# Performance work log

Measured on AMD Instinct MI355X. Metric: run time of the kernel, lower is better.

Reference implementation:

```python
import jax, jax.numpy as jnp
from jax import lax
import numpy as np

B, T, I, H, C = 32, 256, 128, 128, 100


def setup_inputs() -> dict:
    key = jax.random.key(0)
    ks = jax.random.split(key, 9)
    s = 1.0 / np.sqrt(H)  # PyTorch LSTMCell init range
    inp = {
        "x": jax.random.normal(ks[0], (B, T, I), dtype=jnp.float32),
        "w_ih": jax.random.uniform(ks[1], (4 * H, I), jnp.float32, -s, s),
        "b_ih": jax.random.uniform(ks[2], (4 * H,), jnp.float32, -s, s),
        "w_hh": jax.random.uniform(ks[3], (4 * H, H), jnp.float32, -s, s),
        "b_hh": jax.random.uniform(ks[4], (4 * H,), jnp.float32, -s, s),
        # attention params: normal(mean=0, std=0.01) per the source
        "w1": 0.01 * jax.random.normal(ks[5], (2 * H, H), dtype=jnp.float32),
        "w2": 0.01 * jax.random.normal(ks[6], (H, 1), dtype=jnp.float32),
        "w_fc": jax.random.uniform(ks[7], (C, H), jnp.float32, -s, s),
        "b_fc": jax.random.uniform(ks[8], (C,), jnp.float32, -s, s),
    }
    return inp


def _forward(x, w_ih, b_ih, w_hh, b_hh, w1, w2, w_fc, b_fc):
    Bv, Tv, _ = x.shape
    Hv = w_hh.shape[1]
    h0 = jnp.zeros((Bv, Hv), x.dtype)
    c0 = jnp.zeros((Bv, Hv), x.dtype)
    # memory buffer: slot 0 holds the initial zero hidden state (as in the
    # torch code, h_old starts as h_t=0); slots 1..T filled as we go.
    # Unwritten (future) slots are zero, so their attn contribution
    # attn_w * h_old is exactly zero -> no mask needed, matching the
    # growing-memory semantics of the original loop.
    mem0 = jnp.zeros((Bv, Tv + 1, Hv), x.dtype)
    attn0 = jnp.zeros((Bv, Hv), x.dtype)

    def step(carry, inp):
        h, c, mem, _ = carry
        x_t, i = inp
        # PyTorch LSTMCell: gate order i, f, g, o
        gates = x_t @ w_ih.T + b_ih + h @ w_hh.T + b_hh
        ig, fg, gg, og = jnp.split(gates, 4, axis=-1)
        c = jax.nn.sigmoid(fg) * c + jax.nn.sigmoid(ig) * jnp.tanh(gg)
        h = jax.nn.sigmoid(og) * jnp.tanh(c)
        # additive attention scores over the memory (NO softmax in source)
        h_rep = jnp.broadcast_to(h[:, None, :], mem.shape)  # [B, T+1, H]
        cat = jnp.concatenate([h_rep, mem], axis=-1)        # [B, T+1, 2H]
        s = jnp.tanh(cat @ w1) @ w2                          # [B, T+1, 1]
        attn_c = jnp.sum(s * mem, axis=1)                    # [B, H]
        mem = mem.at[:, i + 1, :].set(h)  # append h_t to memory
        return (h, c, mem, attn_c), None

    xs = (jnp.transpose(x, (1, 0, 2)), jnp.arange(Tv))
    (h, c, mem, attn_c), _ = lax.scan(step, (h0, c0, mem0, attn0), xs)
    return (h + attn_c) @ w_fc.T + b_fc


def reference(x, w_ih, b_ih, w_hh, b_hh, w1, w2, w_fc, b_fc):
    return _forward(x, w_ih, b_ih, w_hh, b_hh, w1, w2, w_fc, b_fc)
```

## Files before the change

kernel.cpp:

```cpp
#include <hip/hip_runtime.h>
#include <hip/hip_bf16.h>


#define Bsz 32
#define Tsz 256
#define Isz 128
#define Hsz 128
#define Csz 100
#define G4H 512

typedef short v8s __attribute__((ext_vector_type(8)));
typedef float v4fa __attribute__((ext_vector_type(4)));

__device__ __forceinline__ float2 pk_fma(float2 a, float2 b, float2 c) {
    float2 d;
    asm("v_pk_fma_f32 %0, %1, %2, %3" : "=v"(d) : "v"(a), "v"(b), "v"(c));
    return d;
}
__device__ __forceinline__ float quad_rsum(float x) {
    int t = __builtin_amdgcn_update_dpp(0, __float_as_int(x), 0xB1, 0xF, 0xF, true);
    x += __int_as_float(t);
    t = __builtin_amdgcn_update_dpp(0, __float_as_int(x), 0x4E, 0xF, 0xF, true);
    x += __int_as_float(t);
    return x;
}
__device__ __forceinline__ float rcpf(float x) { return __builtin_amdgcn_rcpf(x); }
__device__ __forceinline__ float sigm_n(float x) { return rcpf(1.0f + __expf(-x)); }
__device__ __forceinline__ float tanh_n(float x) {
    float ax = fabsf(x);
    float e = __expf(-2.0f * ax);
    float t = (1.0f - e) * rcpf(1.0f + e);
    return copysignf(t, x);
}
__device__ __forceinline__ float tanh_s(float x) { return tanh_n(x); }
__device__ __forceinline__ short bf16_bits(float x) {
    __hip_bfloat16 h = __float2bfloat16(x);
    return *reinterpret_cast<short*>(&h);
}
__device__ __forceinline__ float bf16_val(float x) {
    return __bfloat162float(__float2bfloat16(x));
}

__global__ __launch_bounds__(256) void prep_kernel(
    const float* __restrict__ w_ih, const float* __restrict__ b_ih,
    const float* __restrict__ w_hh, const float* __restrict__ b_hh,
    const float* __restrict__ w1,
    __hip_bfloat16* __restrict__ W2ih, __hip_bfloat16* __restrict__ W2v,
    float* __restrict__ whh_pk, float* __restrict__ bias,
    float* __restrict__ attn_c) {
    int idx = blockIdx.x * blockDim.x + threadIdx.x;
    if (idx < G4H * Isz) {
        int n = idx >> 7;
        int k = idx & 127;
        float x = w_ih[idx];
        __hip_bfloat16 hi = __float2bfloat16(x);
        __hip_bfloat16 lo = __float2bfloat16(x - __bfloat162float(hi));
        W2ih[(size_t)n * 384 + k] = hi;
        W2ih[(size_t)n * 384 + 128 + k] = lo;
        W2ih[(size_t)n * 384 + 256 + k] = hi;

        int j4  = idx & 3;
        int q   = (idx >> 2) & 3;
        int d   = (idx >> 4) & 127;
        int gi  = (idx >> 11) & 3;
        int kk4 = (idx >> 13) & 7;
        whh_pk[idx] = w_hh[(size_t)((gi << 7) + d) * 128 + (q << 5) + (kk4 << 2) + j4];
    }
    if (idx < Hsz * Hsz) {
        int n = idx >> 7;
        int k = idx & 127;
        float x = w1[(size_t)(128 + k) * Hsz + n];
        __hip_bfloat16 hi = __float2bfloat16(x);
        __hip_bfloat16 lo = __float2bfloat16(x - __bfloat162float(hi));
        W2v[(size_t)n * 384 + k] = hi;
        W2v[(size_t)n * 384 + 128 + k] = lo;
        W2v[(size_t)n * 384 + 256 + k] = hi;
    }
    if (idx < G4H) bias[idx] = b_ih[idx] + b_hh[idx];
    if (idx < Bsz * Hsz) attn_c[idx] = 0.0f;
}

__global__ __launch_bounds__(256) void gemm_mfma_f32a(
    const float* __restrict__ A, const __hip_bfloat16* __restrict__ W2,
    const float* __restrict__ bias, float* __restrict__ C, int M, int N) {
    const int tid = threadIdx.x;
    const int w = tid >> 6, lane = tid & 63;
    const int m0 = blockIdx.y * 64 + (w & 1) * 32;
    const int n0 = blockIdx.x * 64 + (w >> 1) * 32;
    const int r = lane & 15, quad = lane >> 4;

    v8s Ahi[2][4], Alo[2][4];
    #pragma unroll
    for (int i = 0; i < 2; ++i)
        #pragma unroll
        for (int cb = 0; cb < 4; ++cb) {
            const float* src = A + (size_t)(m0 + 16 * i + r) * Isz + cb * 32 + quad * 8;
            float4 f0 = *(const float4*)src;
            float4 f1 = *(const float4*)(src + 4);
            float f[8] = {f0.x, f0.y, f0.z, f0.w, f1.x, f1.y, f1.z, f1.w};
            v8s hi, lo;
            #pragma unroll
            for (int e = 0; e < 8; ++e) {
                float hv = bf16_val(f[e]);
                hi[e] = bf16_bits(f[e]);
                lo[e] = bf16_bits(f[e] - hv);
            }
            Ahi[i][cb] = hi;
            Alo[i][cb] = lo;
        }

    v4fa acc[2][2] = {};
    const short* Wb = (const short*)W2;
    #pragma unroll
    for (int ks = 0; ks < 12; ++ks) {
        int cb = ks & 3;
        v8s a0 = (ks >= 8) ? Alo[0][cb] : Ahi[0][cb];
        v8s a1 = (ks >= 8) ? Alo[1][cb] : Ahi[1][cb];
        int kb = ks * 32 + quad * 8;
        v8s b0 = *(const v8s*)(Wb + (size_t)(n0 + r) * 384 + kb);
        v8s b1 = *(const v8s*)(Wb + (size_t)(n0 + 16 + r) * 384 + kb);
        acc[0][0] = __builtin_amdgcn_mfma_f32_16x16x32_bf16(a0, b0, acc[0][0], 0, 0, 0);
        acc[0][1] = __builtin_amdgcn_mfma_f32_16x16x32_bf16(a0, b1, acc[0][1], 0, 0, 0);
        acc[1][0] = __builtin_amdgcn_mfma_f32_16x16x32_bf16(a1, b0, acc[1][0], 0, 0, 0);
        acc[1][1] = __builtin_amdgcn_mfma_f32_16x16x32_bf16(a1, b1, acc[1][1], 0, 0, 0);
    }
    #pragma unroll
    for (int i = 0; i < 2; ++i)
        #pragma unroll
        for (int j = 0; j < 2; ++j) {
            int cn = n0 + 16 * j + r;
            float bb = bias ? bias[cn] : 0.0f;
            #pragma unroll
            for (int rr = 0; rr < 4; ++rr) {
                int row = m0 + 16 * i + quad * 4 + rr;
                C[(size_t)row * N + cn] = acc[i][j][rr] + bb;
            }
        }
}

#define HPAD(k) ((k) + 8 * ((k) >> 5))

__global__ __launch_bounds__(512, 2) void lstm_seq(
    const float* __restrict__ G, const float* __restrict__ whh_pk,
    float* __restrict__ H_all) {
    const int b = blockIdx.x;
    const int tid = threadIdx.x;
    const int d = tid >> 2;
    const int q = tid & 3;

    __shared__ float h_s[2][160];

    float2 w2v[4][16];
    {
        const float4* wp = (const float4*)whh_pk;
        #pragma unroll
        for (int kk4 = 0; kk4 < 8; ++kk4)
            #pragma unroll
            for (int gi = 0; gi < 4; ++gi) {
                float4 v = wp[((kk4 * 4 + gi) * 128 + d) * 4 + q];
                w2v[gi][kk4 * 2]     = make_float2(v.x, v.y);
                w2v[gi][kk4 * 2 + 1] = make_float2(v.z, v.w);
            }
    }

    if (tid < 320) ((float*)h_s)[tid] = 0.0f;
    float c = 0.0f;
    __syncthreads();

    const float* Gq = G + (size_t)b * Tsz * G4H + q * 128 + d;
    float* Hst = H_all + (size_t)b * Tsz * Hsz + d;

    float gval = Gq[0];
    int cur = 0;
    for (int t = 0; t < Tsz; ++t) {
        const int tn = (t < Tsz - 1) ? t + 1 : t;
        float ngval = Gq[(size_t)tn * G4H];

        float2 accA[4], accB[4];
        #pragma unroll
        for (int gi = 0; gi < 4; ++gi) {
            accA[gi] = make_float2(q == gi ? gval : 0.f, 0.f);
            accB[gi] = make_float2(0.f, 0.f);
        }
        const float4* hb4 = (const float4*)&h_s[cur][q * 40];
        #pragma unroll
        for (int kk4 = 0; kk4 < 8; ++kk4) {
            float4 h4 = hb4[kk4];
            float2 hA = make_float2(h4.x, h4.y);
            float2 hB = make_float2(h4.z, h4.w);
            accA[0] = pk_fma(hA, w2v[0][2 * kk4], accA[0]);
            accA[1] = pk_fma(hA, w2v[1][2 * kk4], accA[1]);
            accA[2] = pk_fma(hA, w2v[2][2 * kk4], accA[2]);
            accA[3] = pk_fma(hA, w2v[3][2 * kk4], accA[3]);
            accB[0] = pk_fma(hB, w2v[0][2 * kk4 + 1], accB[0]);
            accB[1] = pk_fma(hB, w2v[1][2 * kk4 + 1], accB[1]);
            accB[2] = pk_fma(hB, w2v[2][2 * kk4 + 1], accB[2]);
            accB[3] = pk_fma(hB, w2v[3][2 * kk4 + 1], accB[3]);
        }
        float a0 = quad_rsum(accA[0].x + accA[0].y + accB[0].x + accB[0].y);
        float a1 = quad_rsum(accA[1].x + accA[1].y + accB[1].x + accB[1].y);
        float a2 = quad_rsum(accA[2].x + accA[2].y + accB[2].x + accB[2].y);
        float a3 = quad_rsum(accA[3].x + accA[3].y + accB[3].x + accB[3].y);

        float iv = sigm_n(a0);
        float fv = sigm_n(a1);
        float gv = tanh_n(a2);
        float ov = sigm_n(a3);
        c = fv * c + iv * gv;
        float h = ov * tanh_n(c);

        if (q == 0) {
            h_s[cur ^ 1][HPAD(d)] = h;
            Hst[(size_t)t * Hsz] = h;
        }
        gval = ngval;
        __syncthreads();
        cur ^= 1;
    }
}

__global__ __launch_bounds__(256) void scores_part(
    const float* __restrict__ H_all, const float* __restrict__ KV,
    const float* __restrict__ w1, const float* __restrict__ w2,
    float* __restrict__ attn_c) {
    const int b = blockIdx.y, jt = blockIdx.x;
    const int tid = threadIdx.x;
    __shared__ float hT[Hsz];
    __shared__ float q_s[Hsz];
    __shared__ float w2s[Hsz];
    __shared__ float s_s[64];
    __shared__ float part[2][Hsz];

    const float* Hb = H_all + (size_t)b * Tsz * Hsz;
    const float* KVb = KV + (size_t)b * Tsz * Hsz;

    if (tid < Hsz) {
        hT[tid] = Hb[255 * Hsz + tid];
        w2s[tid] = w2[tid];
    }
    __syncthreads();
    if (tid < Hsz) {
        float acc = 0.f;
        #pragma unroll 8
        for (int k = 0; k < Hsz; ++k) acc = fmaf(hT[k], w1[k * Hsz + tid], acc);
        q_s[tid] = acc;
    }
    __syncthreads();

    const int jl = tid >> 2, ql = tid & 3;
    const int j = jt * 64 + jl;
    float p = 0.f;
    if (j < 255) {
        const float* kv = KVb + (size_t)j * Hsz + ql * 32;
        const float* qs = q_s + ql * 32;
        const float* wv = w2s + ql * 32;
        #pragma unroll 8
        for (int k = 0; k < 32; ++k)
            p = fmaf(tanh_s(qs[k] + kv[k]), wv[k], p);
    }
    p = quad_rsum(p);
    if (ql == 0) s_s[jl] = (j < 255) ? p : 0.0f;
    __syncthreads();

    {
        const int dd = tid & 127, half = tid >> 7;
        float acc = 0.f;
        #pragma unroll 4
        for (int u = 0; u < 32; ++u) {
            int lj = half * 32 + u;
            int jj = jt * 64 + lj;
            if (jj < 255) acc = fmaf(s_s[lj], Hb[(size_t)jj * Hsz + dd], acc);
        }
        part[half][dd] = acc;
    }
    __syncthreads();
    if (tid < Hsz) atomicAdd(&attn_c[b * Hsz + tid], part[0][tid] + part[1][tid]);
}

__global__ __launch_bounds__(256) void fc_out(
    const float* __restrict__ H_all, const float* __restrict__ attn_c,
    const float* __restrict__ w_fc, const float* __restrict__ b_fc,
    float* __restrict__ out) {
    const int b = blockIdx.x, tid = threadIdx.x;
    __shared__ float r_s[Hsz];
    if (tid < Hsz)
        r_s[tid] = H_all[(size_t)b * Tsz * Hsz + 255 * Hsz + tid] + attn_c[b * Hsz + tid];
    __syncthreads();
    const int o = tid >> 1, half = tid & 1;
    float acc = 0.f;
    if (o < Csz) {
        const float* wr = w_fc + (size_t)o * Hsz + half * 64;
        const float* rr = r_s + half * 64;
        #pragma unroll 8
        for (int k = 0; k < 64; ++k) acc = fmaf(rr[k], wr[k], acc);
    }
    acc += __shfl_xor(acc, 1);
    if (half == 0 && o < Csz) out[b * Csz + o] = acc + b_fc[o];
}

extern "C" void kernel_launch(void* const* d_in, const int* in_sizes, int n_in,
                              void* d_out, int out_size, void* d_ws, size_t ws_size,
                              hipStream_t stream) {
    const float* x    = (const float*)d_in[0];
    const float* w_ih = (const float*)d_in[1];
    const float* b_ih = (const float*)d_in[2];
    const float* w_hh = (const float*)d_in[3];
    const float* b_hh = (const float*)d_in[4];
    const float* w1   = (const float*)d_in[5];
    const float* w2   = (const float*)d_in[6];
    const float* w_fc = (const float*)d_in[7];
    const float* b_fc = (const float*)d_in[8];

    float* ws = (float*)d_ws;
    float* whh_pk = ws;
    float* bias   = whh_pk + 65536;
    float* attn_c = bias + 512;
    __hip_bfloat16* W2ih = (__hip_bfloat16*)(attn_c + 4096);
    __hip_bfloat16* W2v  = (__hip_bfloat16*)(attn_c + 4096 + 98304);
    float* G      = attn_c + 4096 + 98304 + 24576;
    float* H_all  = G + 4194304;
    float* KV     = H_all + 1048576;

    prep_kernel<<<256, 256, 0, stream>>>(w_ih, b_ih, w_hh, b_hh, w1,
                                         W2ih, W2v, whh_pk, bias, attn_c);

    dim3 gG(G4H / 64, (Bsz * Tsz) / 64);
    gemm_mfma_f32a<<<gG, 256, 0, stream>>>(x, W2ih, bias, G, Bsz * Tsz, G4H);

    lstm_seq<<<Bsz, 512, 0, stream>>>(G, whh_pk, H_all);

    dim3 gK(Hsz / 64, (Bsz * Tsz) / 64);
    gemm_mfma_f32a<<<gK, 256, 0, stream>>>(H_all, W2v, nullptr, KV, Bsz * Tsz, Hsz);

    dim3 gS(4, Bsz);
    scores_part<<<gS, 256, 0, stream>>>(H_all, KV, w1, w2, attn_c);

    fc_out<<<Bsz, 256, 0, stream>>>(H_all, attn_c, w_fc, b_fc, (float*)d_out);
}
```

Measured before the change: 330.7 us.

## Fuse key GEMM, attention scores and output FC into one kernel

Replaces the separate key-projection GEMM, the partial-scores kernel with atomics, and the final FC kernel with a single per-batch kernel. It computes H·W1v with split-bf16 MFMA in registers, applies tanh and w2 directly, then does the weighted sum and FC. This removes two launches, the KV round trip through global memory, the attn_c zeroing and the atomics. The cost is parallelism: only 32 blocks now do all the attention work, and each block re-reads W2v.

```diff
diff --git a/kernel.cpp b/kernel.cpp
--- a/kernel.cpp
+++ b/kernel.cpp
@@ -46,8 +46,7 @@
     const float* __restrict__ w_hh, const float* __restrict__ b_hh,
     const float* __restrict__ w1,
     __hip_bfloat16* __restrict__ W2ih, __hip_bfloat16* __restrict__ W2v,
-    float* __restrict__ whh_pk, float* __restrict__ bias,
-    float* __restrict__ attn_c) {
+    float* __restrict__ whh_pk, float* __restrict__ bias) {
     int idx = blockIdx.x * blockDim.x + threadIdx.x;
     if (idx < G4H * Isz) {
         int n = idx >> 7;
@@ -77,7 +76,6 @@
         W2v[(size_t)n * 384 + 256 + k] = hi;
     }
     if (idx < G4H) bias[idx] = b_ih[idx] + b_hh[idx];
-    if (idx < Bsz * Hsz) attn_c[idx] = 0.0f;
 }
 
 __global__ __launch_bounds__(256) void gemm_mfma_f32a(
@@ -219,20 +217,23 @@
     }
 }
 
-__global__ __launch_bounds__(256) void scores_part(
-    const float* __restrict__ H_all, const float* __restrict__ KV,
+__global__ __launch_bounds__(256) void attn_fused(
+    const float* __restrict__ H_all, const __hip_bfloat16* __restrict__ W2v,
     const float* __restrict__ w1, const float* __restrict__ w2,
-    float* __restrict__ attn_c) {
-    const int b = blockIdx.y, jt = blockIdx.x;
-    const int tid = threadIdx.x;
+    const float* __restrict__ w_fc, const float* __restrict__ b_fc,
+    float* __restrict__ out) {
+    const int b = blockIdx.x, tid = threadIdx.x;
+    const int w = tid >> 6, lane = tid & 63;
+    const int r = lane & 15, quad = lane >> 4;
+
     __shared__ float hT[Hsz];
     __shared__ float q_s[Hsz];
     __shared__ float w2s[Hsz];
-    __shared__ float s_s[64];
+    __shared__ float s_s[Tsz];
     __shared__ float part[2][Hsz];
+    __shared__ float r_s[Hsz];
 
     const float* Hb = H_all + (size_t)b * Tsz * Hsz;
-    const float* KVb = KV + (size_t)b * Tsz * Hsz;
 
     if (tid < Hsz) {
         hT[tid] = Hb[255 * Hsz + tid];
@@ -247,55 +248,88 @@
     }
     __syncthreads();
 
-    const int jl = tid >> 2, ql = tid & 3;
-    const int j = jt * 64 + jl;
-    float p = 0.f;
-    if (j < 255) {
-        const float* kv = KVb + (size_t)j * Hsz + ql * 32;
-        const float* qs = q_s + ql * 32;
-        const float* wv = w2s + ql * 32;
-        #pragma unroll 8
-        for (int k = 0; k < 32; ++k)
-            p = fmaf(tanh_s(qs[k] + kv[k]), wv[k], p);
-    }
-    p = quad_rsum(p);
-    if (ql == 0) s_s[jl] = (j < 255) ? p : 0.0f;
+    const short* Wb = (const short*)W2v;
+    #pragma unroll 1
+    for (int pass = 0; pass < 4; ++pass) {
+        const int jb = pass * 64 + w * 16;
+        v8s Ahi[4], Alo[4];
+        const float* src_base = Hb + (size_t)(jb + r) * Hsz;
+        #pragma unroll
+        for (int cb = 0; cb < 4; ++cb) {
+            const float* src = src_base + cb * 32 + quad * 8;
+            float4 f0 = *(const float4*)src;
+            float4 f1 = *(const float4*)(src + 4);
+            float f[8] = {f0.x, f0.y, f0.z, f0.w, f1.x, f1.y, f1.z, f1.w};
+            v8s hi, lo;
+            #pragma unroll
+            for (int e = 0; e < 8; ++e) {
+                float hv = bf16_val(f[e]);
+                hi[e] = bf16_bits(f[e]);
+                lo[e] = bf16_bits(f[e] - hv);
+            }
+            Ahi[cb] = hi;
+            Alo[cb] = lo;
+        }
+        float p0 = 0.f, p1 = 0.f, p2 = 0.f, p3 = 0.f;
+        #pragma unroll
+        for (int ot = 0; ot < 8; ++ot) {
+            v4fa acc = {};
+            const int n0 = ot * 16;
+            #pragma unroll
+            for (int ks = 0; ks < 12; ++ks) {
+                int cb = ks & 3;
+                v8s a = (ks >= 8) ? Alo[cb] : Ahi[cb];
+                v8s bf = *(const v8s*)(Wb + (size_t)(n0 + r) * 384 + ks * 32 + quad * 8);
+                acc = __builtin_amdgcn_mfma_f32_16x16x32_bf16(a, bf, acc, 0, 0, 0);
+            }
+            const int n = n0 + r;
+            float qn = q_s[n], wn = w2s[n];
+            p0 = fmaf(tanh_s(qn + acc[0]), wn, p0);
+            p1 = fmaf(tanh_s(qn + acc[1]), wn, p1);
+            p2 = fmaf(tanh_s(qn + acc[2]), wn, p2);
+            p3 = fmaf(tanh_s(qn + acc[3]), wn, p3);
+        }
+        #pragma unroll
+        for (int m = 1; m <= 8; m <<= 1) {
+            p0 += __shfl_xor(p0, m);
+            p1 += __shfl_xor(p1, m);
+            p2 += __shfl_xor(p2, m);
+            p3 += __shfl_xor(p3, m);
+        }
+        if (r == 0) {
+            const int j0 = jb + quad * 4;
+            if (j0 + 0 < 255) s_s[j0 + 0] = p0;
+            if (j0 + 1 < 255) s_s[j0 + 1] = p1;
+            if (j0 + 2 < 255) s_s[j0 + 2] = p2;
+            if (j0 + 3 < 255) s_s[j0 + 3] = p3;
+        }
+    }
     __syncthreads();
 
     {
         const int dd = tid & 127, half = tid >> 7;
+        const int j0 = half * 128, je = half ? 255 : 128;
         float acc = 0.f;
         #pragma unroll 4
-        for (int u = 0; u < 32; ++u) {
-            int lj = half * 32 + u;
-            int jj = jt * 64 + lj;
-            if (jj < 255) acc = fmaf(s_s[lj], Hb[(size_t)jj * Hsz + dd], acc);
-        }
+        for (int j = j0; j < je; ++j) acc = fmaf(s_s[j], Hb[(size_t)j * Hsz + dd], acc);
         part[half][dd] = acc;
     }
     __syncthreads();
-    if (tid < Hsz) atomicAdd(&attn_c[b * Hsz + tid], part[0][tid] + part[1][tid]);
-}
-
-__global__ __launch_bounds__(256) void fc_out(
-    const float* __restrict__ H_all, const float* __restrict__ attn_c,
-    const float* __restrict__ w_fc, const float* __restrict__ b_fc,
-    float* __restrict__ out) {
-    const int b = blockIdx.x, tid = threadIdx.x;
-    __shared__ float r_s[Hsz];
-    if (tid < Hsz)
-        r_s[tid] = H_all[(size_t)b * Tsz * Hsz + 255 * Hsz + tid] + attn_c[b * Hsz + tid];
-    __syncthreads();
-    const int o = tid >> 1, half = tid & 1;
-    float acc = 0.f;
-    if (o < Csz) {
-        const float* wr = w_fc + (size_t)o * Hsz + half * 64;
-        const float* rr = r_s + half * 64;
-        #pragma unroll 8
-        for (int k = 0; k < 64; ++k) acc = fmaf(rr[k], wr[k], acc);
-    }
-    acc += __shfl_xor(acc, 1);
-    if (half == 0 && o < Csz) out[b * Csz + o] = acc + b_fc[o];
+    if (tid < Hsz) r_s[tid] = hT[tid] + part[0][tid] + part[1][tid];
+    __syncthreads();
+
+    {
+        const int o = tid >> 1, half = tid & 1;
+        float acc = 0.f;
+        if (o < Csz) {
+            const float* wr = w_fc + (size_t)o * Hsz + half * 64;
+            const float* rr = r_s + half * 64;
+            #pragma unroll 8
+            for (int k = 0; k < 64; ++k) acc = fmaf(rr[k], wr[k], acc);
+        }
+        acc += __shfl_xor(acc, 1);
+        if (half == 0 && o < Csz) out[b * Csz + o] = acc + b_fc[o];
+    }
 }
 
 extern "C" void kernel_launch(void* const* d_in, const int* in_sizes, int n_in,
@@ -314,26 +348,18 @@
     float* ws = (float*)d_ws;
     float* whh_pk = ws;
     float* bias   = whh_pk + 65536;
-    float* attn_c = bias + 512;
-    __hip_bfloat16* W2ih = (__hip_bfloat16*)(attn_c + 4096);
-    __hip_bfloat16* W2v  = (__hip_bfloat16*)(attn_c + 4096 + 98304);
-    float* G      = attn_c + 4096 + 98304 + 24576;
+    __hip_bfloat16* W2ih = (__hip_bfloat16*)(bias + 512);
+    __hip_bfloat16* W2v  = (__hip_bfloat16*)(bias + 512 + 98304);
+    float* G      = bias + 512 + 98304 + 24576;
     float* H_all  = G + 4194304;
-    float* KV     = H_all + 1048576;
 
     prep_kernel<<<256, 256, 0, stream>>>(w_ih, b_ih, w_hh, b_hh, w1,
-                                         W2ih, W2v, whh_pk, bias, attn_c);
+                                         W2ih, W2v, whh_pk, bias);
 
     dim3 gG(G4H / 64, (Bsz * Tsz) / 64);
     gemm_mfma_f32a<<<gG, 256, 0, stream>>>(x, W2ih, bias, G, Bsz * Tsz, G4H);
 
     lstm_seq<<<Bsz, 512, 0, stream>>>(G, whh_pk, H_all);
 
-    dim3 gK(Hsz / 64, (Bsz * Tsz) / 64);
-    gemm_mfma_f32a<<<gK, 256, 0, stream>>>(H_all, W2v, nullptr, KV, Bsz * Tsz, Hsz);
-
-    dim3 gS(4, Bsz);
-    scores_part<<<gS, 256, 0, stream>>>(H_all, KV, w1, w2, attn_c);
-
-    fc_out<<<Bsz, 256, 0, stream>>>(H_all, attn_c, w_fc, b_fc, (float*)d_out);
-}
+    attn_fused<<<Bsz, 256, 0, stream>>>(H_all, W2v, w1, w2, w_fc, b_fc, (float*)d_out);
+}
```

Result: slower. 339.5 us (+2.7%).

## Split LSTM recurrence across 2 lanes per hidden unit instead of 4

Applied to the files above, without the earlier changes.

The recurrent kernel now uses 256 threads per batch row, with two lanes per hidden unit each covering half of the K dimension, instead of 512 threads with four lanes. Each thread holds twice as many W_hh values in registers (128 float2) and does twice the FMAs per step. In return the cross-lane reduction needs one DPP step instead of two, and there are fewer waves to synchronise at each step's barrier. The risk is higher register pressure and a longer serial FMA chain per step, and the removal of LDS padding may introduce bank conflicts.

```diff
diff --git a/kernel.cpp b/kernel.cpp
--- a/kernel.cpp
+++ b/kernel.cpp
@@ -23,6 +23,10 @@
     t = __builtin_amdgcn_update_dpp(0, __float_as_int(x), 0x4E, 0xF, 0xF, true);
     x += __int_as_float(t);
     return x;
+}
+__device__ __forceinline__ float pair_rsum(float x) {
+    int t = __builtin_amdgcn_update_dpp(0, __float_as_int(x), 0xB1, 0xF, 0xF, true);
+    return x + __int_as_float(t);
 }
 __device__ __forceinline__ float rcpf(float x) { return __builtin_amdgcn_rcpf(x); }
 __device__ __forceinline__ float sigm_n(float x) { return rcpf(1.0f + __expf(-x)); }
@@ -59,12 +63,12 @@
         W2ih[(size_t)n * 384 + 128 + k] = lo;
         W2ih[(size_t)n * 384 + 256 + k] = hi;
 
-        int j4  = idx & 3;
-        int q   = (idx >> 2) & 3;
-        int d   = (idx >> 4) & 127;
-        int gi  = (idx >> 11) & 3;
-        int kk4 = (idx >> 13) & 7;
-        whh_pk[idx] = w_hh[(size_t)((gi << 7) + d) * 128 + (q << 5) + (kk4 << 2) + j4];
+        int j   = idx & 1;
+        int t   = (idx >> 1) & 255;
+        int gi  = (idx >> 9) & 3;
+        int kk2 = idx >> 11;
+        int d   = t >> 1, q = t & 1;
+        whh_pk[idx] = w_hh[(size_t)((gi << 7) + d) * 128 + (q << 6) + (kk2 << 1) + j];
     }
     if (idx < Hsz * Hsz) {
         int n = idx >> 7;
@@ -138,53 +142,53 @@
         }
 }
 
-#define HPAD(k) ((k) + 8 * ((k) >> 5))
-
-__global__ __launch_bounds__(512, 2) void lstm_seq(
+__global__ __launch_bounds__(256, 1) void lstm_seq(
     const float* __restrict__ G, const float* __restrict__ whh_pk,
     float* __restrict__ H_all) {
     const int b = blockIdx.x;
     const int tid = threadIdx.x;
-    const int d = tid >> 2;
-    const int q = tid & 3;
-
-    __shared__ float h_s[2][160];
-
-    float2 w2v[4][16];
+    const int d = tid >> 1;
+    const int q = tid & 1;
+
+    __shared__ float h_s[2][Hsz];
+
+    float2 w2v[4][32];
     {
-        const float4* wp = (const float4*)whh_pk;
-        #pragma unroll
-        for (int kk4 = 0; kk4 < 8; ++kk4)
+        const float2* wp = (const float2*)whh_pk;
+        #pragma unroll
+        for (int kk2 = 0; kk2 < 32; ++kk2)
             #pragma unroll
-            for (int gi = 0; gi < 4; ++gi) {
-                float4 v = wp[((kk4 * 4 + gi) * 128 + d) * 4 + q];
-                w2v[gi][kk4 * 2]     = make_float2(v.x, v.y);
-                w2v[gi][kk4 * 2 + 1] = make_float2(v.z, v.w);
-            }
-    }
-
-    if (tid < 320) ((float*)h_s)[tid] = 0.0f;
+            for (int gi = 0; gi < 4; ++gi)
+                w2v[gi][kk2] = wp[(kk2 * 4 + gi) * 256 + tid];
+    }
+
+    if (tid < 2 * Hsz) ((float*)h_s)[tid] = 0.0f;
     float c = 0.0f;
     __syncthreads();
 
-    const float* Gq = G + (size_t)b * Tsz * G4H + q * 128 + d;
+    const float* Gq0 = G + (size_t)b * Tsz * G4H + q * 128 + d;
+    const float* Gq2 = Gq0 + 256;
     float* Hst = H_all + (size_t)b * Tsz * Hsz + d;
 
-    float gval = Gq[0];
+    float g0v = Gq0[0], g2v = Gq2[0];
     int cur = 0;
     for (int t = 0; t < Tsz; ++t) {
         const int tn = (t < Tsz - 1) ? t + 1 : t;
-        float ngval = Gq[(size_t)tn * G4H];
+        float ng0 = Gq0[(size_t)tn * G4H];
+        float ng2 = Gq2[(size_t)tn * G4H];
 
         float2 accA[4], accB[4];
         #pragma unroll
         for (int gi = 0; gi < 4; ++gi) {
-            accA[gi] = make_float2(q == gi ? gval : 0.f, 0.f);
+            accA[gi] = make_float2(0.f, 0.f);
             accB[gi] = make_float2(0.f, 0.f);
         }
-        const float4* hb4 = (const float4*)&h_s[cur][q * 40];
-        #pragma unroll
-        for (int kk4 = 0; kk4 < 8; ++kk4) {
+        accA[q].x = g0v;
+        accA[q + 2].x = g2v;
+
+        const float4* hb4 = (const float4*)&h_s[cur][q * 64];
+        #pragma unroll
+        for (int kk4 = 0; kk4 < 16; ++kk4) {
             float4 h4 = hb4[kk4];
             float2 hA = make_float2(h4.x, h4.y);
             float2 hB = make_float2(h4.z, h4.w);
@@ -197,10 +201,10 @@
             accB[2] = pk_fma(hB, w2v[2][2 * kk4 + 1], accB[2]);
             accB[3] = pk_fma(hB, w2v[3][2 * kk4 + 1], accB[3]);
         }
-        float a0 = quad_rsum(accA[0].x + accA[0].y + accB[0].x + accB[0].y);
-        float a1 = quad_rsum(accA[1].x + accA[1].y + accB[1].x + accB[1].y);
-        float a2 = quad_rsum(accA[2].x + accA[2].y + accB[2].x + accB[2].y);
-        float a3 = quad_rsum(accA[3].x + accA[3].y + accB[3].x + accB[3].y);
+        float a0 = pair_rsum(accA[0].x + accA[0].y + accB[0].x + accB[0].y);
+        float a1 = pair_rsum(accA[1].x + accA[1].y + accB[1].x + accB[1].y);
+        float a2 = pair_rsum(accA[2].x + accA[2].y + accB[2].x + accB[2].y);
+        float a3 = pair_rsum(accA[3].x + accA[3].y + accB[3].x + accB[3].y);
 
         float iv = sigm_n(a0);
         float fv = sigm_n(a1);
@@ -210,10 +214,11 @@
         float h = ov * tanh_n(c);
 
         if (q == 0) {
-            h_s[cur ^ 1][HPAD(d)] = h;
+            h_s[cur ^ 1][d] = h;
             Hst[(size_t)t * Hsz] = h;
         }
-        gval = ngval;
+        g0v = ng0;
+        g2v = ng2;
         __syncthreads();
         cur ^= 1;
     }
@@ -327,7 +332,7 @@
     dim3 gG(G4H / 64, (Bsz * Tsz) / 64);
     gemm_mfma_f32a<<<gG, 256, 0, stream>>>(x, W2ih, bias, G, Bsz * Tsz, G4H);
 
-    lstm_seq<<<Bsz, 512, 0, stream>>>(G, whh_pk, H_all);
+    lstm_seq<<<Bsz, 256, 0, stream>>>(G, whh_pk, H_all);
 
     dim3 gK(Hsz / 64, (Bsz * Tsz) / 64);
     gemm_mfma_f32a<<<gK, 256, 0, stream>>>(H_all, W2v, nullptr, KV, Bsz * Tsz, Hsz);
```

After: 500.1 us. 1.51x slower.

## Split LSTM recurrent dot product 8-way across 1024 threads per batch

Applied to the files above, without the earlier changes.

The sequential LSTM kernel now uses 1024 threads per batch row instead of 512. Each hidden unit's K=128 reduction is split across 8 lanes instead of 4, so every thread holds half as many recurrent weights in registers (16 float4) and runs a shorter FMA chain per timestep. The w_hh repack layout changes to match, and an extra DPP half-mirror step completes the 8-lane reduction. The aim is to shorten each serial step's latency, at the cost of a block-wide barrier over twice as many waves every timestep.

```diff
diff --git a/kernel.cpp b/kernel.cpp
--- a/kernel.cpp
+++ b/kernel.cpp
@@ -21,6 +21,15 @@
     int t = __builtin_amdgcn_update_dpp(0, __float_as_int(x), 0xB1, 0xF, 0xF, true);
     x += __int_as_float(t);
     t = __builtin_amdgcn_update_dpp(0, __float_as_int(x), 0x4E, 0xF, 0xF, true);
+    x += __int_as_float(t);
+    return x;
+}
+__device__ __forceinline__ float oct_rsum(float x) {
+    int t = __builtin_amdgcn_update_dpp(0, __float_as_int(x), 0xB1, 0xF, 0xF, true);
+    x += __int_as_float(t);
+    t = __builtin_amdgcn_update_dpp(0, __float_as_int(x), 0x4E, 0xF, 0xF, true);
+    x += __int_as_float(t);
+    t = __builtin_amdgcn_update_dpp(0, __float_as_int(x), 0x141, 0xF, 0xF, true);
     x += __int_as_float(t);
     return x;
 }
@@ -59,12 +68,12 @@
         W2ih[(size_t)n * 384 + 128 + k] = lo;
         W2ih[(size_t)n * 384 + 256 + k] = hi;
 
-        int j4  = idx & 3;
-        int q   = (idx >> 2) & 3;
-        int d   = (idx >> 4) & 127;
-        int gi  = (idx >> 11) & 3;
-        int kk4 = (idx >> 13) & 7;
-        whh_pk[idx] = w_hh[(size_t)((gi << 7) + d) * 128 + (q << 5) + (kk4 << 2) + j4];
+        int j  = idx & 3;
+        int t  = (idx >> 2) & 1023;
+        int c  = idx >> 12;
+        int d  = t >> 3, q = t & 7;
+        int gi = c & 3, kc = c >> 2;
+        whh_pk[idx] = w_hh[(size_t)((gi << 7) + d) * 128 + (q << 4) + (kc << 2) + j];
     }
     if (idx < Hsz * Hsz) {
         int n = idx >> 7;
@@ -138,69 +147,68 @@
         }
 }
 
-#define HPAD(k) ((k) + 8 * ((k) >> 5))
-
-__global__ __launch_bounds__(512, 2) void lstm_seq(
+__global__ __launch_bounds__(1024, 4) void lstm_seq(
     const float* __restrict__ G, const float* __restrict__ whh_pk,
     float* __restrict__ H_all) {
     const int b = blockIdx.x;
     const int tid = threadIdx.x;
-    const int d = tid >> 2;
-    const int q = tid & 3;
-
-    __shared__ float h_s[2][160];
-
-    float2 w2v[4][16];
-    {
-        const float4* wp = (const float4*)whh_pk;
-        #pragma unroll
-        for (int kk4 = 0; kk4 < 8; ++kk4)
-            #pragma unroll
-            for (int gi = 0; gi < 4; ++gi) {
-                float4 v = wp[((kk4 * 4 + gi) * 128 + d) * 4 + q];
-                w2v[gi][kk4 * 2]     = make_float2(v.x, v.y);
-                w2v[gi][kk4 * 2 + 1] = make_float2(v.z, v.w);
-            }
-    }
-
-    if (tid < 320) ((float*)h_s)[tid] = 0.0f;
+    const int d = tid >> 3;
+    const int q = tid & 7;
+
+    __shared__ float h_s[2][Hsz];
+
+    const float4* wp4 = (const float4*)whh_pk;
+#define WL(c) float4 w##c = wp4[(c) * 1024 + tid];
+    WL(0) WL(1) WL(2) WL(3) WL(4) WL(5) WL(6) WL(7)
+    WL(8) WL(9) WL(10) WL(11) WL(12) WL(13) WL(14) WL(15)
+#undef WL
+
+    if (tid < 2 * Hsz) ((float*)h_s)[tid] = 0.0f;
     float c = 0.0f;
     __syncthreads();
 
     const float* Gq = G + (size_t)b * Tsz * G4H + q * 128 + d;
     float* Hst = H_all + (size_t)b * Tsz * Hsz + d;
 
-    float gval = Gq[0];
+    float gval = (q < 4) ? Gq[0] : 0.0f;
     int cur = 0;
     for (int t = 0; t < Tsz; ++t) {
         const int tn = (t < Tsz - 1) ? t + 1 : t;
-        float ngval = Gq[(size_t)tn * G4H];
-
-        float2 accA[4], accB[4];
-        #pragma unroll
-        for (int gi = 0; gi < 4; ++gi) {
-            accA[gi] = make_float2(q == gi ? gval : 0.f, 0.f);
-            accB[gi] = make_float2(0.f, 0.f);
-        }
-        const float4* hb4 = (const float4*)&h_s[cur][q * 40];
-        #pragma unroll
-        for (int kk4 = 0; kk4 < 8; ++kk4) {
-            float4 h4 = hb4[kk4];
-            float2 hA = make_float2(h4.x, h4.y);
-            float2 hB = make_float2(h4.z, h4.w);
-            accA[0] = pk_fma(hA, w2v[0][2 * kk4], accA[0]);
-            accA[1] = pk_fma(hA, w2v[1][2 * kk4], accA[1]);
-            accA[2] = pk_fma(hA, w2v[2][2 * kk4], accA[2]);
-            accA[3] = pk_fma(hA, w2v[3][2 * kk4], accA[3]);
-            accB[0] = pk_fma(hB, w2v[0][2 * kk4 + 1], accB[0]);
-            accB[1] = pk_fma(hB, w2v[1][2 * kk4 + 1], accB[1]);
-            accB[2] = pk_fma(hB, w2v[2][2 * kk4 + 1], accB[2]);
-            accB[3] = pk_fma(hB, w2v[3][2 * kk4 + 1], accB[3]);
-        }
-        float a0 = quad_rsum(accA[0].x + accA[0].y + accB[0].x + accB[0].y);
-        float a1 = quad_rsum(accA[1].x + accA[1].y + accB[1].x + accB[1].y);
-        float a2 = quad_rsum(accA[2].x + accA[2].y + accB[2].x + accB[2].y);
-        float a3 = quad_rsum(accA[3].x + accA[3].y + accB[3].x + accB[3].y);
+        float ngval = (q < 4) ? Gq[(size_t)tn * G4H] : 0.0f;
+
+        float s0 = (q == 0) ? gval : 0.f;
+        float s1 = (q == 1) ? gval : 0.f;
+        float s2 = (q == 2) ? gval : 0.f;
+        float s3 = (q == 3) ? gval : 0.f;
+        float2 A0 = make_float2(s0, 0.f), B0 = make_float2(0.f, 0.f);
+        float2 A1 = make_float2(s1, 0.f), B1 = make_float2(0.f, 0.f);
+        float2 A2 = make_float2(s2, 0.f), B2 = make_float2(0.f, 0.f);
+        float2 A3 = make_float2(s3, 0.f), B3 = make_float2(0.f, 0.f);
+
+        const float4* hb4 = (const float4*)&h_s[cur][q * 16];
+        float4 h0 = hb4[0], h1 = hb4[1], h2 = hb4[2], h3 = hb4[3];
+
+#define KCBLK(h4, g0, g1, g2, g3) { \
+        float2 hA = make_float2(h4.x, h4.y), hB = make_float2(h4.z, h4.w); \
+        A0 = pk_fma(hA, make_float2(g0.x, g0.y), A0); \
+        B0 = pk_fma(hB, make_float2(g0.z, g0.w), B0); \
+        A1 = pk_fma(hA, make_float2(g1.x, g1.y), A1); \
+        B1 = pk_fma(hB, make_float2(g1.z, g1.w), B1); \
+        A2 = pk_fma(hA, make_float2(g2.x, g2.y), A2); \
+        B2 = pk_fma(hB, make_float2(g2.z, g2.w), B2); \
+        A3 = pk_fma(hA, make_float2(g3.x, g3.y), A3); \
+        B3 = pk_fma(hB, make_float2(g3.z, g3.w), B3); }
+
+        KCBLK(h0, w0, w1, w2, w3)
+        KCBLK(h1, w4, w5, w6, w7)
+        KCBLK(h2, w8, w9, w10, w11)
+        KCBLK(h3, w12, w13, w14, w15)
+#undef KCBLK
+
+        float a0 = oct_rsum(A0.x + A0.y + B0.x + B0.y);
+        float a1 = oct_rsum(A1.x + A1.y + B1.x + B1.y);
+        float a2 = oct_rsum(A2.x + A2.y + B2.x + B2.y);
+        float a3 = oct_rsum(A3.x + A3.y + B3.x + B3.y);
 
         float iv = sigm_n(a0);
         float fv = sigm_n(a1);
@@ -210,7 +218,7 @@
         float h = ov * tanh_n(c);
 
         if (q == 0) {
-            h_s[cur ^ 1][HPAD(d)] = h;
+            h_s[cur ^ 1][d] = h;
             Hst[(size_t)t * Hsz] = h;
         }
         gval = ngval;
@@ -327,7 +335,7 @@
     dim3 gG(G4H / 64, (Bsz * Tsz) / 64);
     gemm_mfma_f32a<<<gG, 256, 0, stream>>>(x, W2ih, bias, G, Bsz * Tsz, G4H);
 
-    lstm_seq<<<Bsz, 512, 0, stream>>>(G, whh_pk, H_all);
+    lstm_seq<<<Bsz, 1024, 0, stream>>>(G, whh_pk, H_all);
 
     dim3 gK(Hsz / 64, (Bsz * Tsz) / 64);
     gemm_mfma_f32a<<<gK, 256, 0, stream>>>(H_all, W2v, nullptr, KV, Bsz * Tsz, Hsz);
```

Result: slower. 443.0 us (+34.0%).
